# Kernel tuning notes

Measured on AMD Instinct MI355X. Metric: run time of the kernel, lower is better.

Reference implementation:

```python
import jax, jax.numpy as jnp
import numpy as np

H = 8  # GRU hidden size (Dimension)


def _gru_last_hidden(x, Wih, Whh, bih, bhh):
    """Torch-style GRU (batch_first), returns final hidden state [B, H].
    x: [B, T, In]; Wih: [3H, In]; Whh: [3H, H]; bih, bhh: [3H].
    Gate order (torch): r, z, n.
    """
    B = x.shape[0]
    # precompute input projections for all timesteps: [B, T, 3H]
    xg = jnp.einsum('bti,gi->btg', x, Wih) + bih

    def step(h, xt):  # h: [B,H], xt: [B,3H]
        gh = h @ Whh.T + bhh  # [B, 3H]
        xr, xz, xn = jnp.split(xt, 3, axis=-1)
        hr, hz, hn = jnp.split(gh, 3, axis=-1)
        r = jax.nn.sigmoid(xr + hr)
        z = jax.nn.sigmoid(xz + hz)
        n = jnp.tanh(xn + r * hn)
        h_new = (1.0 - z) * n + z * h
        return h_new, None

    h0 = jnp.zeros((B, H), dtype=x.dtype)
    hT, _ = jax.lax.scan(step, h0, jnp.swapaxes(xg, 0, 1))  # scan over T
    return hT


def setup_inputs() -> dict:
    key = jax.random.key(0)
    ks = jax.random.split(key, 10)
    B, T = 1024, 512
    s = 0.2  # param init scale ~ 1/sqrt(H)*... small
    return {
        'bbox': jax.random.normal(ks[0], (B, T, 4), dtype=jnp.float32),
        'flow': jax.random.normal(ks[1], (B, T, 5, 5, 2), dtype=jnp.float32),
        'Wih_b': jax.random.normal(ks[2], (3 * H, 4), dtype=jnp.float32) * s,
        'Whh_b': jax.random.normal(ks[3], (3 * H, H), dtype=jnp.float32) * s,
        'bih_b': jax.random.normal(ks[4], (3 * H,), dtype=jnp.float32) * s,
        'bhh_b': jax.random.normal(ks[5], (3 * H,), dtype=jnp.float32) * s,
        'Wih_f': jax.random.normal(ks[6], (3 * H, 2), dtype=jnp.float32) * s,
        'Whh_f': jax.random.normal(ks[7], (3 * H, H), dtype=jnp.float32) * s,
        'bih_f': jax.random.normal(ks[8], (3 * H,), dtype=jnp.float32) * s,
        'bhh_f': jax.random.normal(ks[9], (3 * H,), dtype=jnp.float32) * s,
    }


def reference(bbox, flow, Wih_b, Whh_b, bih_b, bhh_b, Wih_f, Whh_f, bih_f, bhh_f):
    # vectorized equivalent of the triple Python loop: take center pixel
    storage = flow[:, :, 2, 2, :]  # [B, T, 2]
    h_bbox = _gru_last_hidden(bbox, Wih_b, Whh_b, bih_b, bhh_b)      # [B, H]
    h_flow = _gru_last_hidden(storage, Wih_f, Whh_f, bih_f, bhh_f)   # [B, H]
    feature = (h_bbox + h_flow) * 0.5
    return feature
```

## Files before the change

### kernel.cpp

```cpp
#include <hip/hip_runtime.h>

#define HDIM 8
#define CHUNK 16

typedef float v4f __attribute__((ext_vector_type(4)));
typedef float v2f __attribute__((ext_vector_type(2)));

__device__ __forceinline__ float ex2(float x) {
#if __has_builtin(__builtin_amdgcn_exp2f)
    return __builtin_amdgcn_exp2f(x);
#else
    return exp2f(x);
#endif
}
__device__ __forceinline__ float rcp(float x) {
#if __has_builtin(__builtin_amdgcn_rcpf)
    return __builtin_amdgcn_rcpf(x);
#else
    return 1.0f / x;
#endif
}

#define DPP_ROR(v, N)                                                        \
    __int_as_float(__builtin_amdgcn_update_dpp(                              \
        0, __float_as_int(v), 0x120 + (N), 0xF, 0xF, true))


#define KEEPALIVE16(a)                                                       \
    asm volatile("" : "+v"(a##0), "+v"(a##1), "+v"(a##2), "+v"(a##3),        \
                      "+v"(a##4), "+v"(a##5), "+v"(a##6), "+v"(a##7),        \
                      "+v"(a##8), "+v"(a##9), "+v"(a##10), "+v"(a##11),      \
                      "+v"(a##12), "+v"(a##13), "+v"(a##14), "+v"(a##15))

template <int IN, int STRIDE>
__device__ __forceinline__ void produce_chunk(
    const float* __restrict__ xb, int t0,
    const float (&ur)[4], const float (&uz)[4], const float (&un)[4],
    float cr, float cz, float cn,
    float4* __restrict__ dst, int lane)
{
    const float* bp = xb + (size_t)t0 * STRIDE;
#define PLOAD4(i) v4f x##i = *reinterpret_cast<const v4f*>(bp + (i) * STRIDE);
#define PLOAD2(i) v2f x##i = *reinterpret_cast<const v2f*>(bp + (i) * STRIDE);
#define PSTORE(i)                                                            \
    {                                                                        \
        float a = cr, b = cz, c = cn;                                        \
        _Pragma("unroll")                                                    \
        for (int i2 = 0; i2 < IN; ++i2) {                                    \
            a = fmaf(ur[i2], x##i[i2], a);                                   \
            b = fmaf(uz[i2], x##i[i2], b);                                   \
            c = fmaf(un[i2], x##i[i2], c);                                   \
        }                                                                    \
        dst[(i) * 64 + lane] = make_float4(a, b, c, 0.0f);                   \
    }
    if constexpr (IN == 4) {
        PLOAD4(0) PLOAD4(1) PLOAD4(2) PLOAD4(3) PLOAD4(4) PLOAD4(5)
        PLOAD4(6) PLOAD4(7) PLOAD4(8) PLOAD4(9) PLOAD4(10) PLOAD4(11)
        PLOAD4(12) PLOAD4(13) PLOAD4(14) PLOAD4(15)
        KEEPALIVE16(x);
        PSTORE(0) PSTORE(1) PSTORE(2) PSTORE(3) PSTORE(4) PSTORE(5)
        PSTORE(6) PSTORE(7) PSTORE(8) PSTORE(9) PSTORE(10) PSTORE(11)
        PSTORE(12) PSTORE(13) PSTORE(14) PSTORE(15)
    } else {
        PLOAD2(0) PLOAD2(1) PLOAD2(2) PLOAD2(3) PLOAD2(4) PLOAD2(5)
        PLOAD2(6) PLOAD2(7) PLOAD2(8) PLOAD2(9) PLOAD2(10) PLOAD2(11)
        PLOAD2(12) PLOAD2(13) PLOAD2(14) PLOAD2(15)
        KEEPALIVE16(x);
        PSTORE(0) PSTORE(1) PSTORE(2) PSTORE(3) PSTORE(4) PSTORE(5)
        PSTORE(6) PSTORE(7) PSTORE(8) PSTORE(9) PSTORE(10) PSTORE(11)
        PSTORE(12) PSTORE(13) PSTORE(14) PSTORE(15)
    }
#undef PLOAD4
#undef PLOAD2
#undef PSTORE
}

__device__ __forceinline__ float consume_chunk(
    float hj, const float4* __restrict__ src, int lane,
    const float (&wr)[8], const float (&wz)[8], const float (&wn)[8], float bhn)
{
    const v4f* sp = reinterpret_cast<const v4f*>(src);
#define CLOAD(i) v4f p##i = sp[(i) * 64 + lane];
    CLOAD(0) CLOAD(1) CLOAD(2) CLOAD(3) CLOAD(4) CLOAD(5) CLOAD(6) CLOAD(7)
    CLOAD(8) CLOAD(9) CLOAD(10) CLOAD(11) CLOAD(12) CLOAD(13) CLOAD(14) CLOAD(15)
    KEEPALIVE16(p);
#undef CLOAD

#define FMAC3(ROT, M)                                                        \
    "v_fmac_f32_dpp %[ar], %[h], %[wr" #M "] row_ror:" #ROT                  \
    " row_mask:0xf bank_mask:0xf\n\t"                                        \
    "v_fmac_f32_dpp %[az], %[h], %[wz" #M "] row_ror:" #ROT                  \
    " row_mask:0xf bank_mask:0xf\n\t"                                        \
    "v_fmac_f32_dpp %[an], %[h], %[wn" #M "] row_ror:" #ROT                  \
    " row_mask:0xf bank_mask:0xf\n\t"

#define STEP(P)                                                              \
    {                                                                        \
        float ar = fmaf(wr[0], hj, (P).x);                                   \
        float az = fmaf(wz[0], hj, (P).y);                                   \
        float an_ = fmaf(wn[0], hj, bhn);                                    \
        asm volatile(                                                        \
            FMAC3(2, 1) FMAC3(4, 2) FMAC3(6, 3) FMAC3(8, 4)                  \
            FMAC3(10, 5) FMAC3(12, 6) FMAC3(14, 7)                           \
            : [ar] "+v"(ar), [az] "+v"(az), [an] "+v"(an_)                   \
            : [h] "v"(hj),                                                   \
              [wr1] "v"(wr[1]), [wz1] "v"(wz[1]), [wn1] "v"(wn[1]),          \
              [wr2] "v"(wr[2]), [wz2] "v"(wz[2]), [wn2] "v"(wn[2]),          \
              [wr3] "v"(wr[3]), [wz3] "v"(wz[3]), [wn3] "v"(wn[3]),          \
              [wr4] "v"(wr[4]), [wz4] "v"(wz[4]), [wn4] "v"(wn[4]),          \
              [wr5] "v"(wr[5]), [wz5] "v"(wz[5]), [wn5] "v"(wn[5]),          \
              [wr6] "v"(wr[6]), [wz6] "v"(wz[6]), [wn6] "v"(wn[6]),          \
              [wr7] "v"(wr[7]), [wz7] "v"(wz[7]), [wn7] "v"(wn[7]));         \
        float r = rcp(1.0f + ex2(ar));                                       \
        float z = rcp(1.0f + ex2(az));                                       \
        float u = fmaf(r, an_, (P).z);                                       \
        float n = fmaf(-2.0f, rcp(1.0f + ex2(u)), 1.0f);                     \
        hj = fmaf(z, hj - n, n);                                             \
    }
    STEP(p0) STEP(p1) STEP(p2) STEP(p3) STEP(p4) STEP(p5) STEP(p6) STEP(p7)
    STEP(p8) STEP(p9) STEP(p10) STEP(p11) STEP(p12) STEP(p13) STEP(p14) STEP(p15)
#undef STEP
#undef FMAC3
    return hj;
}

__global__ __launch_bounds__(256, 1)
void gru_fused_kernel(const float* __restrict__ bbox, const float* __restrict__ flow,
                      const float* __restrict__ Wih_b, const float* __restrict__ Whh_b,
                      const float* __restrict__ bih_b, const float* __restrict__ bhh_b,
                      const float* __restrict__ Wih_f, const float* __restrict__ Whh_f,
                      const float* __restrict__ bih_f, const float* __restrict__ bhh_f,
                      float* __restrict__ out, int T)
{
    const float NL2E = -1.4426950408889634f;
    const float L2E2 =  2.8853900817779268f;

    __shared__ float4 projLDS[2][2][CHUNK * 64];
    __shared__ float sh[2][8][HDIM];

    const int tid  = threadIdx.x;
    const int wave = tid >> 6;
    const int lane = tid & 63;
    const int gru  = wave & 1;
    const bool is_cons = (wave < 2);
    const int NC = T / CHUNK;

    const int eloc = ((lane >> 4) << 1) | (lane & 1);
    const int j    = (lane & 15) >> 1;

    float wr[8], wz[8], wn[8];
    float bhn = 0.0f;
    float ur[4] = {0, 0, 0, 0}, uz[4] = {0, 0, 0, 0}, un[4] = {0, 0, 0, 0};
    float cr = 0.0f, cz = 0.0f, cn = 0.0f;
    const float* pxb = nullptr;

    if (is_cons) {
        const float* Whh = gru ? Whh_f : Whh_b;
        const float* bhh = gru ? bhh_f : bhh_b;
        float nbp = DPP_ROR((float)j, 2);
        const int dstep = (nbp == (float)((j + 1) & 7)) ? 1 : 7;
#pragma unroll
        for (int m = 0; m < 8; ++m) {
            const int k = (j + dstep * m) & 7;
            wr[m] = NL2E * Whh[(j     ) * HDIM + k];
            wz[m] = NL2E * Whh[(j +  8) * HDIM + k];
            wn[m] = L2E2 * Whh[(j + 16) * HDIM + k];
        }
        bhn = L2E2 * bhh[j + 16];
    } else {
        const float* Wih = gru ? Wih_f : Wih_b;
        const float* bih = gru ? bih_f : bih_b;
        const float* bhh = gru ? bhh_f : bhh_b;
        const int IN = gru ? 2 : 4;
        const int pe = blockIdx.x * 8 + eloc;
        pxb = gru ? (flow + (size_t)pe * T * 50 + 24)
                  : (bbox + (size_t)pe * T * 4);
        for (int i = 0; i < IN; ++i) {
            ur[i] = NL2E * Wih[(j     ) * IN + i];
            uz[i] = NL2E * Wih[(j +  8) * IN + i];
            un[i] = L2E2 * Wih[(j + 16) * IN + i];
        }
        cr = NL2E * (bih[j]     + bhh[j]);
        cz = NL2E * (bih[j + 8] + bhh[j + 8]);
        cn = L2E2 * bih[j + 16];
    }

    float hj = 0.0f;

    if (!is_cons) {
        float4* dst = projLDS[0][gru];
        if (gru == 0) produce_chunk<4, 4 >(pxb, 0, ur, uz, un, cr, cz, cn, dst, lane);
        else          produce_chunk<2, 50>(pxb, 0, ur, uz, un, cr, cz, cn, dst, lane);
    }
    __syncthreads();

    for (int c = 0; c < NC; ++c) {
        if (is_cons) {
            hj = consume_chunk(hj, projLDS[c & 1][gru], lane, wr, wz, wn, bhn);
        } else if (c + 1 < NC) {
            float4* dst = projLDS[(c + 1) & 1][gru];
            if (gru == 0) produce_chunk<4, 4 >(pxb, (c + 1) * CHUNK, ur, uz, un, cr, cz, cn, dst, lane);
            else          produce_chunk<2, 50>(pxb, (c + 1) * CHUNK, ur, uz, un, cr, cz, cn, dst, lane);
        }
        __syncthreads();
    }

    if (is_cons) sh[gru][eloc][j] = hj;
    __syncthreads();
    if (wave == 0) {
        const int e = blockIdx.x * 8 + eloc;
        out[(size_t)e * HDIM + j] = 0.5f * (sh[0][eloc][j] + sh[1][eloc][j]);
    }
}

extern "C" void kernel_launch(void* const* d_in, const int* in_sizes, int n_in,
                              void* d_out, int out_size, void* d_ws, size_t ws_size,
                              hipStream_t stream) {
    const float* bbox  = (const float*)d_in[0];
    const float* flow  = (const float*)d_in[1];
    const float* Wih_b = (const float*)d_in[2];
    const float* Whh_b = (const float*)d_in[3];
    const float* bih_b = (const float*)d_in[4];
    const float* bhh_b = (const float*)d_in[5];
    const float* Wih_f = (const float*)d_in[6];
    const float* Whh_f = (const float*)d_in[7];
    const float* bih_f = (const float*)d_in[8];
    const float* bhh_f = (const float*)d_in[9];
    float* out = (float*)d_out;

    const int B = out_size / HDIM;
    const int T = in_sizes[0] / (4 * B);

    dim3 grid(B / 8), block(256);
    gru_fused_kernel<<<grid, block, 0, stream>>>(
        bbox, flow, Wih_b, Whh_b, bih_b, bhh_b,
        Wih_f, Whh_f, bih_f, bhh_f, out, T);
}
```

Before: 56.83 us.

## Interleave two independent GRU recurrences per consumer lane to hide latency

Each consumer lane now advances two batch elements' hidden states at once, interleaving their DPP matvec and transcendental chains so one recurrence's dependency latency overlaps the other's. The block handles 16 elements instead of 8, so the grid is halved, and the chunk size drops to 8 to keep register and LDS use in check. Each gate's 8-term dot product is split into two partial sums to shorten the dependency chain, and the gate math is rearranged with explicit inline asm ordering. The trade-off is half as many blocks, which on a many-CU GPU may leave compute units idle, plus more barrier syncs per timestep.

```diff
diff --git a/kernel.cpp b/kernel.cpp
--- a/kernel.cpp
+++ b/kernel.cpp
@@ -1,7 +1,7 @@
 #include <hip/hip_runtime.h>
 
 #define HDIM 8
-#define CHUNK 16
+#define CHUNK 8
 
 typedef float v4f __attribute__((ext_vector_type(4)));
 typedef float v2f __attribute__((ext_vector_type(2)));
@@ -25,15 +25,77 @@
     __int_as_float(__builtin_amdgcn_update_dpp(                              \
         0, __float_as_int(v), 0x120 + (N), 0xF, 0xF, true))
 
+#define ASM_FMA(d, a, b, c)                                                  \
+    asm volatile("v_fma_f32 %0, %1, %2, %3"                                  \
+                 : "=v"(d) : "v"(a), "v"(b), "v"(c))
+#define ASM_MULD(d, h, w, ROT)                                               \
+    asm volatile("v_mul_f32_dpp %0, %1, %2 row_ror:" #ROT                    \
+                 " row_mask:0xf bank_mask:0xf"                               \
+                 : "=v"(d) : "v"(h), "v"(w))
+#define ASM_FMACD(d, h, w, ROT)                                              \
+    asm volatile("v_fmac_f32_dpp %0, %1, %2 row_ror:" #ROT                   \
+                 " row_mask:0xf bank_mask:0xf"                               \
+                 : "+v"(d) : "v"(h), "v"(w))
 
 #define KEEPALIVE16(a)                                                       \
     asm volatile("" : "+v"(a##0), "+v"(a##1), "+v"(a##2), "+v"(a##3),        \
                       "+v"(a##4), "+v"(a##5), "+v"(a##6), "+v"(a##7),        \
                       "+v"(a##8), "+v"(a##9), "+v"(a##10), "+v"(a##11),      \
                       "+v"(a##12), "+v"(a##13), "+v"(a##14), "+v"(a##15))
+#define KEEPALIVE8(a)                                                        \
+    asm volatile("" : "+v"(a##0), "+v"(a##1), "+v"(a##2), "+v"(a##3),        \
+                      "+v"(a##4), "+v"(a##5), "+v"(a##6), "+v"(a##7))
+
+__device__ __forceinline__ void gru_step2(
+    float& hjA, float& hjB, v4f PA, v4f PB,
+    const float (&wr)[8], const float (&wz)[8], const float (&wn)[8], float bhn)
+{
+    float raA, rbA, naA, nbA, zaA, zbA;
+    float raB, rbB, naB, nbB, zaB, zbB;
+    ASM_FMA (raA, wr[0], hjA, PA.x);  ASM_FMA (raB, wr[0], hjB, PB.x);
+    ASM_FMA (naA, wn[0], hjA, bhn);   ASM_FMA (naB, wn[0], hjB, bhn);
+    ASM_MULD(rbA, hjA, wr[4], 8);     ASM_MULD(rbB, hjB, wr[4], 8);
+    ASM_MULD(nbA, hjA, wn[4], 8);     ASM_MULD(nbB, hjB, wn[4], 8);
+    ASM_FMACD(raA, hjA, wr[1], 2);    ASM_FMACD(raB, hjB, wr[1], 2);
+    ASM_FMACD(naA, hjA, wn[1], 2);    ASM_FMACD(naB, hjB, wn[1], 2);
+    ASM_FMACD(rbA, hjA, wr[5], 10);   ASM_FMACD(rbB, hjB, wr[5], 10);
+    ASM_FMACD(nbA, hjA, wn[5], 10);   ASM_FMACD(nbB, hjB, wn[5], 10);
+    ASM_FMACD(raA, hjA, wr[2], 4);    ASM_FMACD(raB, hjB, wr[2], 4);
+    ASM_FMACD(naA, hjA, wn[2], 4);    ASM_FMACD(naB, hjB, wn[2], 4);
+    ASM_FMACD(rbA, hjA, wr[6], 12);   ASM_FMACD(rbB, hjB, wr[6], 12);
+    ASM_FMACD(nbA, hjA, wn[6], 12);   ASM_FMACD(nbB, hjB, wn[6], 12);
+    ASM_FMACD(raA, hjA, wr[3], 6);    ASM_FMACD(raB, hjB, wr[3], 6);
+    ASM_FMACD(naA, hjA, wn[3], 6);    ASM_FMACD(naB, hjB, wn[3], 6);
+    ASM_FMACD(rbA, hjA, wr[7], 14);   ASM_FMACD(rbB, hjB, wr[7], 14);
+    ASM_FMACD(nbA, hjA, wn[7], 14);   ASM_FMACD(nbB, hjB, wn[7], 14);
+    const float arA = raA + rbA,  arB = raB + rbB;
+    const float ErA = ex2(arA),   ErB = ex2(arB);
+    ASM_FMA (zaA, wz[0], hjA, PA.y);  ASM_FMA (zaB, wz[0], hjB, PB.y);
+    ASM_MULD(zbA, hjA, wz[4], 8);     ASM_MULD(zbB, hjB, wz[4], 8);
+    ASM_FMACD(zaA, hjA, wz[1], 2);    ASM_FMACD(zaB, hjB, wz[1], 2);
+    ASM_FMACD(zbA, hjA, wz[5], 10);   ASM_FMACD(zbB, hjB, wz[5], 10);
+    ASM_FMACD(zaA, hjA, wz[2], 4);    ASM_FMACD(zaB, hjB, wz[2], 4);
+    ASM_FMACD(zbA, hjA, wz[6], 12);   ASM_FMACD(zbB, hjB, wz[6], 12);
+    ASM_FMACD(zaA, hjA, wz[3], 6);    ASM_FMACD(zaB, hjB, wz[3], 6);
+    ASM_FMACD(zbA, hjA, wz[7], 14);   ASM_FMACD(zbB, hjB, wz[7], 14);
+    const float anA = naA + nbA,      anB = naB + nbB;
+    const float rA  = rcp(1.0f + ErA), rB = rcp(1.0f + ErB);
+    const float azA = zaA + zbA,      azB = zaB + zbB;
+    const float EzA = ex2(azA),       EzB = ex2(azB);
+    const float uA  = fmaf(rA, anA, PA.z), uB = fmaf(rB, anB, PB.z);
+    const float EnA = ex2(uA),        EnB = ex2(uB);
+    const float zA  = rcp(1.0f + EzA), zB = rcp(1.0f + EzB);
+    const float qA  = zA * hjA,       qB  = zB * hjB;
+    const float ozA = EzA * zA,       ozB = EzB * zB;
+    const float s1A = qA + ozA,       s1B = qB + ozB;
+    const float m2oA = -2.0f * ozA,   m2oB = -2.0f * ozB;
+    const float rnA = rcp(1.0f + EnA), rnB = rcp(1.0f + EnB);
+    hjA = fmaf(rnA, m2oA, s1A);
+    hjB = fmaf(rnB, m2oB, s1B);
+}
 
 template <int IN, int STRIDE>
-__device__ __forceinline__ void produce_chunk(
+__device__ __forceinline__ void produce_chunk8(
     const float* __restrict__ xb, int t0,
     const float (&ur)[4], const float (&uz)[4], const float (&un)[4],
     float cr, float cz, float cn,
@@ -54,74 +116,46 @@
         dst[(i) * 64 + lane] = make_float4(a, b, c, 0.0f);                   \
     }
     if constexpr (IN == 4) {
-        PLOAD4(0) PLOAD4(1) PLOAD4(2) PLOAD4(3) PLOAD4(4) PLOAD4(5)
-        PLOAD4(6) PLOAD4(7) PLOAD4(8) PLOAD4(9) PLOAD4(10) PLOAD4(11)
-        PLOAD4(12) PLOAD4(13) PLOAD4(14) PLOAD4(15)
-        KEEPALIVE16(x);
-        PSTORE(0) PSTORE(1) PSTORE(2) PSTORE(3) PSTORE(4) PSTORE(5)
-        PSTORE(6) PSTORE(7) PSTORE(8) PSTORE(9) PSTORE(10) PSTORE(11)
-        PSTORE(12) PSTORE(13) PSTORE(14) PSTORE(15)
+        PLOAD4(0) PLOAD4(1) PLOAD4(2) PLOAD4(3)
+        PLOAD4(4) PLOAD4(5) PLOAD4(6) PLOAD4(7)
+        KEEPALIVE8(x);
+        PSTORE(0) PSTORE(1) PSTORE(2) PSTORE(3)
+        PSTORE(4) PSTORE(5) PSTORE(6) PSTORE(7)
     } else {
-        PLOAD2(0) PLOAD2(1) PLOAD2(2) PLOAD2(3) PLOAD2(4) PLOAD2(5)
-        PLOAD2(6) PLOAD2(7) PLOAD2(8) PLOAD2(9) PLOAD2(10) PLOAD2(11)
-        PLOAD2(12) PLOAD2(13) PLOAD2(14) PLOAD2(15)
-        KEEPALIVE16(x);
-        PSTORE(0) PSTORE(1) PSTORE(2) PSTORE(3) PSTORE(4) PSTORE(5)
-        PSTORE(6) PSTORE(7) PSTORE(8) PSTORE(9) PSTORE(10) PSTORE(11)
-        PSTORE(12) PSTORE(13) PSTORE(14) PSTORE(15)
+        PLOAD2(0) PLOAD2(1) PLOAD2(2) PLOAD2(3)
+        PLOAD2(4) PLOAD2(5) PLOAD2(6) PLOAD2(7)
+        KEEPALIVE8(x);
+        PSTORE(0) PSTORE(1) PSTORE(2) PSTORE(3)
+        PSTORE(4) PSTORE(5) PSTORE(6) PSTORE(7)
     }
 #undef PLOAD4
 #undef PLOAD2
 #undef PSTORE
 }
 
-__device__ __forceinline__ float consume_chunk(
-    float hj, const float4* __restrict__ src, int lane,
+__device__ __forceinline__ void consume_chunk8(
+    float& hjA, float& hjB,
+    const float4* __restrict__ srcA, const float4* __restrict__ srcB, int lane,
     const float (&wr)[8], const float (&wz)[8], const float (&wn)[8], float bhn)
 {
-    const v4f* sp = reinterpret_cast<const v4f*>(src);
-#define CLOAD(i) v4f p##i = sp[(i) * 64 + lane];
-    CLOAD(0) CLOAD(1) CLOAD(2) CLOAD(3) CLOAD(4) CLOAD(5) CLOAD(6) CLOAD(7)
-    CLOAD(8) CLOAD(9) CLOAD(10) CLOAD(11) CLOAD(12) CLOAD(13) CLOAD(14) CLOAD(15)
-    KEEPALIVE16(p);
-#undef CLOAD
-
-#define FMAC3(ROT, M)                                                        \
-    "v_fmac_f32_dpp %[ar], %[h], %[wr" #M "] row_ror:" #ROT                  \
-    " row_mask:0xf bank_mask:0xf\n\t"                                        \
-    "v_fmac_f32_dpp %[az], %[h], %[wz" #M "] row_ror:" #ROT                  \
-    " row_mask:0xf bank_mask:0xf\n\t"                                        \
-    "v_fmac_f32_dpp %[an], %[h], %[wn" #M "] row_ror:" #ROT                  \
-    " row_mask:0xf bank_mask:0xf\n\t"
-
-#define STEP(P)                                                              \
-    {                                                                        \
-        float ar = fmaf(wr[0], hj, (P).x);                                   \
-        float az = fmaf(wz[0], hj, (P).y);                                   \
-        float an_ = fmaf(wn[0], hj, bhn);                                    \
-        asm volatile(                                                        \
-            FMAC3(2, 1) FMAC3(4, 2) FMAC3(6, 3) FMAC3(8, 4)                  \
-            FMAC3(10, 5) FMAC3(12, 6) FMAC3(14, 7)                           \
-            : [ar] "+v"(ar), [az] "+v"(az), [an] "+v"(an_)                   \
-            : [h] "v"(hj),                                                   \
-              [wr1] "v"(wr[1]), [wz1] "v"(wz[1]), [wn1] "v"(wn[1]),          \
-              [wr2] "v"(wr[2]), [wz2] "v"(wz[2]), [wn2] "v"(wn[2]),          \
-              [wr3] "v"(wr[3]), [wz3] "v"(wz[3]), [wn3] "v"(wn[3]),          \
-              [wr4] "v"(wr[4]), [wz4] "v"(wz[4]), [wn4] "v"(wn[4]),          \
-              [wr5] "v"(wr[5]), [wz5] "v"(wz[5]), [wn5] "v"(wn[5]),          \
-              [wr6] "v"(wr[6]), [wz6] "v"(wz[6]), [wn6] "v"(wn[6]),          \
-              [wr7] "v"(wr[7]), [wz7] "v"(wz[7]), [wn7] "v"(wn[7]));         \
-        float r = rcp(1.0f + ex2(ar));                                       \
-        float z = rcp(1.0f + ex2(az));                                       \
-        float u = fmaf(r, an_, (P).z);                                       \
-        float n = fmaf(-2.0f, rcp(1.0f + ex2(u)), 1.0f);                     \
-        hj = fmaf(z, hj - n, n);                                             \
-    }
-    STEP(p0) STEP(p1) STEP(p2) STEP(p3) STEP(p4) STEP(p5) STEP(p6) STEP(p7)
-    STEP(p8) STEP(p9) STEP(p10) STEP(p11) STEP(p12) STEP(p13) STEP(p14) STEP(p15)
-#undef STEP
-#undef FMAC3
-    return hj;
+    const v4f* sA = reinterpret_cast<const v4f*>(srcA);
+    const v4f* sB = reinterpret_cast<const v4f*>(srcB);
+#define CLA(i)    v4f q##i = sA[(i) * 64 + lane];
+#define CLB(i, k) v4f q##i = sB[(k) * 64 + lane];
+    CLA(0) CLA(1) CLA(2) CLA(3) CLA(4) CLA(5) CLA(6) CLA(7)
+    CLB(8, 0) CLB(9, 1) CLB(10, 2) CLB(11, 3)
+    CLB(12, 4) CLB(13, 5) CLB(14, 6) CLB(15, 7)
+    KEEPALIVE16(q);
+#undef CLA
+#undef CLB
+    gru_step2(hjA, hjB, q0, q8,  wr, wz, wn, bhn);
+    gru_step2(hjA, hjB, q1, q9,  wr, wz, wn, bhn);
+    gru_step2(hjA, hjB, q2, q10, wr, wz, wn, bhn);
+    gru_step2(hjA, hjB, q3, q11, wr, wz, wn, bhn);
+    gru_step2(hjA, hjB, q4, q12, wr, wz, wn, bhn);
+    gru_step2(hjA, hjB, q5, q13, wr, wz, wn, bhn);
+    gru_step2(hjA, hjB, q6, q14, wr, wz, wn, bhn);
+    gru_step2(hjA, hjB, q7, q15, wr, wz, wn, bhn);
 }
 
 __global__ __launch_bounds__(256, 1)
@@ -135,8 +169,8 @@
     const float NL2E = -1.4426950408889634f;
     const float L2E2 =  2.8853900817779268f;
 
-    __shared__ float4 projLDS[2][2][CHUNK * 64];
-    __shared__ float sh[2][8][HDIM];
+    __shared__ float4 projLDS[2][2][2][CHUNK * 64];
+    __shared__ float sh[2][16][HDIM];
 
     const int tid  = threadIdx.x;
     const int wave = tid >> 6;
@@ -147,12 +181,15 @@
 
     const int eloc = ((lane >> 4) << 1) | (lane & 1);
     const int j    = (lane & 15) >> 1;
+    const int eA   = blockIdx.x * 16 + eloc;
+    const int eB   = eA + 8;
 
     float wr[8], wz[8], wn[8];
     float bhn = 0.0f;
     float ur[4] = {0, 0, 0, 0}, uz[4] = {0, 0, 0, 0}, un[4] = {0, 0, 0, 0};
     float cr = 0.0f, cz = 0.0f, cn = 0.0f;
-    const float* pxb = nullptr;
+    const float* pxA = nullptr;
+    const float* pxB = nullptr;
 
     if (is_cons) {
         const float* Whh = gru ? Whh_f : Whh_b;
@@ -172,9 +209,10 @@
         const float* bih = gru ? bih_f : bih_b;
         const float* bhh = gru ? bhh_f : bhh_b;
         const int IN = gru ? 2 : 4;
-        const int pe = blockIdx.x * 8 + eloc;
-        pxb = gru ? (flow + (size_t)pe * T * 50 + 24)
-                  : (bbox + (size_t)pe * T * 4);
+        pxA = gru ? (flow + (size_t)eA * T * 50 + 24)
+                  : (bbox + (size_t)eA * T * 4);
+        pxB = gru ? (flow + (size_t)eB * T * 50 + 24)
+                  : (bbox + (size_t)eB * T * 4);
         for (int i = 0; i < IN; ++i) {
             ur[i] = NL2E * Wih[(j     ) * IN + i];
             uz[i] = NL2E * Wih[(j +  8) * IN + i];
@@ -185,31 +223,49 @@
         cn = L2E2 * bih[j + 16];
     }
 
-    float hj = 0.0f;
+    float hjA = 0.0f, hjB = 0.0f;
 
     if (!is_cons) {
-        float4* dst = projLDS[0][gru];
-        if (gru == 0) produce_chunk<4, 4 >(pxb, 0, ur, uz, un, cr, cz, cn, dst, lane);
-        else          produce_chunk<2, 50>(pxb, 0, ur, uz, un, cr, cz, cn, dst, lane);
+        float4* dA = &projLDS[0][gru][0][0];
+        float4* dB = &projLDS[0][gru][1][0];
+        if (gru == 0) {
+            produce_chunk8<4, 4 >(pxA, 0, ur, uz, un, cr, cz, cn, dA, lane);
+            produce_chunk8<4, 4 >(pxB, 0, ur, uz, un, cr, cz, cn, dB, lane);
+        } else {
+            produce_chunk8<2, 50>(pxA, 0, ur, uz, un, cr, cz, cn, dA, lane);
+            produce_chunk8<2, 50>(pxB, 0, ur, uz, un, cr, cz, cn, dB, lane);
+        }
     }
     __syncthreads();
 
     for (int c = 0; c < NC; ++c) {
         if (is_cons) {
-            hj = consume_chunk(hj, projLDS[c & 1][gru], lane, wr, wz, wn, bhn);
+            consume_chunk8(hjA, hjB,
+                           &projLDS[c & 1][gru][0][0], &projLDS[c & 1][gru][1][0],
+                           lane, wr, wz, wn, bhn);
         } else if (c + 1 < NC) {
-            float4* dst = projLDS[(c + 1) & 1][gru];
-            if (gru == 0) produce_chunk<4, 4 >(pxb, (c + 1) * CHUNK, ur, uz, un, cr, cz, cn, dst, lane);
-            else          produce_chunk<2, 50>(pxb, (c + 1) * CHUNK, ur, uz, un, cr, cz, cn, dst, lane);
+            float4* dA = &projLDS[(c + 1) & 1][gru][0][0];
+            float4* dB = &projLDS[(c + 1) & 1][gru][1][0];
+            const int t0 = (c + 1) * CHUNK;
+            if (gru == 0) {
+                produce_chunk8<4, 4 >(pxA, t0, ur, uz, un, cr, cz, cn, dA, lane);
+                produce_chunk8<4, 4 >(pxB, t0, ur, uz, un, cr, cz, cn, dB, lane);
+            } else {
+                produce_chunk8<2, 50>(pxA, t0, ur, uz, un, cr, cz, cn, dA, lane);
+                produce_chunk8<2, 50>(pxB, t0, ur, uz, un, cr, cz, cn, dB, lane);
+            }
         }
         __syncthreads();
     }
 
-    if (is_cons) sh[gru][eloc][j] = hj;
+    if (is_cons) {
+        sh[gru][eloc][j]     = hjA;
+        sh[gru][eloc + 8][j] = hjB;
+    }
     __syncthreads();
     if (wave == 0) {
-        const int e = blockIdx.x * 8 + eloc;
-        out[(size_t)e * HDIM + j] = 0.5f * (sh[0][eloc][j] + sh[1][eloc][j]);
+        out[(size_t)eA * HDIM + j] = 0.5f * (sh[0][eloc][j]     + sh[1][eloc][j]);
+        out[(size_t)eB * HDIM + j] = 0.5f * (sh[0][eloc + 8][j] + sh[1][eloc + 8][j]);
     }
 }
 
@@ -231,7 +287,7 @@
     const int B = out_size / HDIM;
     const int T = in_sizes[0] / (4 * B);
 
-    dim3 grid(B / 8), block(256);
+    dim3 grid(B / 16), block(256);
     gru_fused_kernel<<<grid, block, 0, stream>>>(
         bbox, flow, Wih_b, Whh_b, bih_b, bhh_b,
         Wih_f, Whh_f, bih_f, bhh_f, out, T);
```

Result: slower. 107.3 us (+88.8%).
